# Kernel tuning notes

Measured on AMD Instinct MI355X. Metric: run time of the kernel, lower is better.

The kernel has to match this reference:

```python
import jax, jax.numpy as jnp
import numpy as np

B, N, DIM = 4, 2048, 768
H, C = 12, 64            # num_heads, head_dim
M = 384                  # num random features = dim * kernel_ratio
SCALE = C ** (-0.25)
EPS = 1e-8
INV_SQRT_M = 1.0 / np.sqrt(M).astype(np.float32)


def _make_orf(key):
    # per-head orthogonal random features: rows of each (C, M) block are
    # orthonormal (C <= M), scaled by sqrt(M), matching sample_orf's intent.
    g = jax.random.normal(key, (H, M, C), jnp.float32)
    q = jnp.linalg.qr(g)[0]                 # (H, M, C), orthonormal columns
    return jnp.transpose(q, (0, 2, 1)) * np.float32(np.sqrt(M))  # (H, C, M)


def setup_inputs() -> dict:
    key = jax.random.key(0)
    k0, k1, k2, k3 = jax.random.split(key, 4)
    x = jax.random.normal(k0, (B, N, DIM), jnp.float32)
    w = _make_orf(k1)                                       # (H, C, M), frozen
    Wqkv = jax.random.normal(k2, (DIM, 3 * DIM), jnp.float32) * 0.02
    Wproj = jax.random.normal(k3, (DIM, DIM), jnp.float32) * 0.02
    bproj = jnp.zeros((DIM,), jnp.float32)
    return {"x": x, "w": w, "Wqkv": Wqkv, "Wproj": Wproj, "bproj": bproj}


def _kernel(x, w):
    # x: (B, H, N, C) -> phi(x): (B, H, N, M)
    xs = x * SCALE
    proj = jnp.einsum('bhnc,hcm->bhnm', xs, w)
    sq_half = 0.5 * jnp.sum(xs * xs, axis=-1, keepdims=True)  # (B,H,N,1)
    return jnp.exp(proj - sq_half) * INV_SQRT_M


def reference(x, w, Wqkv, Wproj, bproj):
    qkv = (x @ Wqkv).reshape(B, N, 3, H, C).transpose(2, 0, 3, 1, 4)
    q, k, v = qkv[0], qkv[1], qkv[2]
    qf = _kernel(q, w)                       # (B, H, N, M)
    kf = _kernel(k, w)                       # (B, H, N, M)
    # normalizer D_n = q'_n . sum_j k'_j
    D = jnp.einsum('bhnm,bhm->bhn', qf, jnp.sum(kf, axis=2)) + EPS
    # linear attention: (k'^T v) then q' @ (k'^T v)
    ktv = jnp.einsum('bhnm,bhnc->bhmc', kf, v)      # (B, H, M, C)
    out = jnp.einsum('bhnm,bhmc->bhnc', qf, ktv) / D[..., None]
    out = out.transpose(0, 2, 1, 3).reshape(B, N, DIM)
    return out @ Wproj + bproj
```

## Files before the change

### kernel.cpp

```cpp
#include <hip/hip_runtime.h>

typedef __attribute__((ext_vector_type(8))) short s16x8;
typedef __attribute__((ext_vector_type(4))) float f32x4;

#define MFMA(a, b, c) __builtin_amdgcn_mfma_f32_16x16x32_bf16(a, b, c, 0, 0, 0)

namespace {

constexpr int Bn = 4, Nn = 2048, Hn = 12, Mn = 384;
constexpr float SCALE = 0.35355339059327379f;
constexpr float ISM = 0.05103103630798288f;
constexpr float EPS = 1e-8f;

__device__ inline unsigned short f2b(float f) {
  unsigned u = __builtin_bit_cast(unsigned, f);
  return (unsigned short)((u + 0x7fffu + ((u >> 16) & 1u)) >> 16);
}
__device__ inline float b2f(unsigned short h) {
  unsigned u = ((unsigned)h) << 16;
  return __builtin_bit_cast(float, u);
}

__device__ inline void gl_lds16(const unsigned short* g, unsigned short* l) {
  __builtin_amdgcn_global_load_lds(
      (const __attribute__((address_space(1))) unsigned int*)g,
      (__attribute__((address_space(3))) unsigned int*)l, 16, 0, 0);
}

__global__ __launch_bounds__(256) void cvt_all_k(const float* __restrict__ x,
                                                 const float* __restrict__ Wqkv,
                                                 const float* __restrict__ Wproj,
                                                 const float* __restrict__ w,
                                                 unsigned short* __restrict__ xb,
                                                 unsigned short* __restrict__ wqT,
                                                 unsigned short* __restrict__ wpT,
                                                 unsigned short* __restrict__ wt) {
  const int bid = blockIdx.x;
  if (bid < 3072) {
    const int id = bid * 256 + threadIdx.x;
    const float* src = x + (size_t)id * 8;
    s16x8 o;
#pragma unroll
    for (int j = 0; j < 8; ++j) o[j] = (short)f2b(src[j]);
    *(s16x8*)(xb + (size_t)id * 8) = o;
  } else if (bid < 3936) {
    const int id = (bid - 3072) * 256 + threadIdx.x;
    const int n = id / 96, kc = (id % 96) * 8;
    s16x8 o;
#pragma unroll
    for (int j = 0; j < 8; ++j) o[j] = (short)f2b(Wqkv[(size_t)(kc + j) * 2304 + n]);
    *(s16x8*)(wqT + (size_t)n * 768 + kc) = o;
  } else if (bid < 4224) {
    const int id = (bid - 3936) * 256 + threadIdx.x;
    const int n = id / 96, kc = (id % 96) * 8;
    s16x8 o;
#pragma unroll
    for (int j = 0; j < 8; ++j) o[j] = (short)f2b(Wproj[(size_t)(kc + j) * 768 + n]);
    *(s16x8*)(wpT + (size_t)n * 768 + kc) = o;
  } else {
    const int id = (bid - 4224) * 256 + threadIdx.x;
    const int h = id / (384 * 8);
    const int r = id % (384 * 8);
    const int m = r / 8, cc = (r % 8) * 8;
    s16x8 o;
#pragma unroll
    for (int j = 0; j < 8; ++j) o[j] = (short)f2b(w[((size_t)h * 64 + cc + j) * 384 + m]);
    *(s16x8*)(wt + ((size_t)h * 384 + m) * 64 + cc) = o;
  }
}

template <bool BF16OUT>
__global__ __launch_bounds__(256) void gemm_bt_k(const unsigned short* __restrict__ A,
                                                 const unsigned short* __restrict__ Bt,
                                                 int Ktot, int ldOut,
                                                 unsigned short* __restrict__ obf,
                                                 float* __restrict__ of32,
                                                 const float* __restrict__ bias) {
  __shared__ unsigned short ldsA[2][128 * 64];
  __shared__ unsigned short ldsB[2][128 * 64];
  const int t = threadIdx.x, lane = t & 63, w = t >> 6;
  const int ln = lane & 15, kg = lane >> 4;
  const size_t bm = (size_t)blockIdx.y * 128, bn = (size_t)blockIdx.x * 128;
  const int wr = w >> 1, wc = w & 1;
  const int sr = lane >> 3, s = lane & 7;
  f32x4 acc[4][4];
#pragma unroll
  for (int i = 0; i < 4; ++i)
#pragma unroll
    for (int j = 0; j < 4; ++j) acc[i][j] = (f32x4){0.f, 0.f, 0.f, 0.f};

  auto stage = [&](int kb, int d) {
#pragma unroll
    for (int c = 0; c < 4; ++c) {
      const int row = c * 32 + w * 8 + sr;
      const int ss = (s ^ (row & 7)) * 8;
      gl_lds16(A + (bm + row) * 768 + kb + ss, &ldsA[d][(c * 4 + w) * 512]);
      gl_lds16(Bt + (bn + row) * 768 + kb + ss, &ldsB[d][(c * 4 + w) * 512]);
    }
  };

  const int nt = Ktot / 64;
  stage(0, 0);
  for (int ti = 0; ti < nt; ++ti) {
    const int cur = ti & 1;
    __syncthreads();
    if (ti + 1 < nt) stage((ti + 1) * 64, cur ^ 1);
    const char* lA = (const char*)ldsA[cur];
    const char* lB = (const char*)ldsB[cur];
#pragma unroll
    for (int ks = 0; ks < 2; ++ks) {
      s16x8 af[4], bfr[4];
#pragma unroll
      for (int mi = 0; mi < 4; ++mi) {
        const int row = wr * 64 + mi * 16 + ln;
        af[mi] = *(const s16x8*)(lA + row * 128 + (((ks * 4 + kg) ^ (row & 7)) << 4));
      }
#pragma unroll
      for (int ni = 0; ni < 4; ++ni) {
        const int row = wc * 64 + ni * 16 + ln;
        bfr[ni] = *(const s16x8*)(lB + row * 128 + (((ks * 4 + kg) ^ (row & 7)) << 4));
      }
#pragma unroll
      for (int mi = 0; mi < 4; ++mi)
#pragma unroll
        for (int ni = 0; ni < 4; ++ni) acc[mi][ni] = MFMA(af[mi], bfr[ni], acc[mi][ni]);
    }
  }
#pragma unroll
  for (int mi = 0; mi < 4; ++mi)
#pragma unroll
    for (int ni = 0; ni < 4; ++ni) {
      const size_t orow0 = bm + wr * 64 + mi * 16 + kg * 4;
      const size_t ocol = bn + wc * 64 + ni * 16 + ln;
#pragma unroll
      for (int r = 0; r < 4; ++r) {
        const float v = acc[mi][ni][r];
        if (BF16OUT)
          obf[(orow0 + r) * ldOut + ocol] = f2b(v);
        else
          of32[(orow0 + r) * ldOut + ocol] = v + bias[ocol];
      }
    }
}

template <int NCT, int CT0>
__device__ inline void s2_gemm2(const char* kfT_b, const char* vt_b, int mts, int ln, int kg,
                                f32x4 (*acc)[3]) {
#pragma unroll
  for (int half = 0; half < 2; ++half) {
    s16x8 a[3], bb[NCT];
#pragma unroll
    for (int j = 0; j < 3; ++j) {
      const int m = (mts + j) * 16 + ln;
      a[j] = *(const s16x8*)(kfT_b + m * 128 + ((half * 64 + kg * 16) ^ ((m & 7) << 4)));
    }
#pragma unroll
    for (int i = 0; i < NCT; ++i) {
      const int c = (CT0 + i) * 16 + ln;
      bb[i] = *(const s16x8*)(vt_b + c * 128 + ((half * 64 + kg * 16) ^ ((c & 7) << 4)));
    }
#pragma unroll
    for (int j = 0; j < 3; ++j)
#pragma unroll
      for (int i = 0; i < NCT; ++i) acc[j][i] = MFMA(a[j], bb[i], acc[j][i]);
  }
}

__global__ __launch_bounds__(512, 4) void stage2_k(const unsigned short* __restrict__ qkv,
                                                   const unsigned short* __restrict__ wt,
                                                   float* __restrict__ ktv_part,
                                                   float* __restrict__ ksum_part) {
  __shared__ unsigned short kfT[192 * 64];
  __shared__ unsigned short vt[80 * 64];
  __shared__ unsigned short wt_s[192 * 64];
  __shared__ unsigned short k_s[64 * 64];
  __shared__ float sqh[64];
  char* kfT_b = (char*)kfT;
  char* vt_b = (char*)vt;
  char* wt_b = (char*)wt_s;
  char* k_b = (char*)k_s;
  const int t = threadIdx.x, lane = t & 63, w = t >> 6;
  const int ln = lane & 15, kg = lane >> 4;
  const int gx = blockIdx.x, h = blockIdx.y, b = blockIdx.z;
  const int ng = gx >> 1, mh = gx & 1, m0 = mh * 192;
  const int bh = b * Hn + h;
  const int ntile = w & 3, mgrp = w >> 2;
  const int mts = (w & 3) * 3;
  const int cg = w >> 2;
  const int lr = lane >> 3, sl = lane & 7;

  auto stage_k = [&](int ch) {
    const int row = w * 8 + lr;
    gl_lds16(qkv + ((size_t)b * Nn + ng * 512 + ch * 64 + row) * 2304 + 768 + h * 64 +
                 ((sl ^ (row & 7)) * 8),
             k_s + w * 512);
  };
  const int vn = t >> 3, vc0 = (t & 7) * 8;
  auto load_v = [&](int ch) {
    return *(const s16x8*)(qkv + ((size_t)b * Nn + ng * 512 + ch * 64 + vn) * 2304 + 1536 +
                           h * 64 + vc0);
  };
  auto scat_v = [&](s16x8 vv) {
#pragma unroll
    for (int j = 0; j < 8; ++j) {
      const int c = vc0 + j;
      *(unsigned short*)(vt_b + c * 128 + ((2 * vn) ^ ((c & 7) << 4))) = (unsigned short)vv[j];
    }
  };
  auto do_sq = [&]() {
    const int n = t >> 3, slq = t & 7;
    const s16x8 kk = *(const s16x8*)(k_b + n * 128 + ((slq ^ (n & 7)) << 4));
    float sacc = 0.f;
#pragma unroll
    for (int j = 0; j < 8; ++j) {
      const float f = b2f((unsigned short)kk[j]);
      sacc = fmaf(f, f, sacc);
    }
    sacc += __shfl_xor(sacc, 1);
    sacc += __shfl_xor(sacc, 2);
    sacc += __shfl_xor(sacc, 4);
    if ((t & 7) == 0) sqh[n] = 0.5f * SCALE * SCALE * sacc;
  };

#pragma unroll
  for (int rr = 0; rr < 3; ++rr) {
    const int j = w * 3 + rr;
    const int row = j * 8 + lr;
    gl_lds16(wt + ((size_t)h * 384 + m0 + row) * 64 + ((sl ^ (row & 7)) * 8), wt_s + j * 512);
  }
  for (int i = t; i < 1024; i += 512) {
    const int c = 64 + (i >> 6), nn = i & 63;
    *(unsigned short*)(vt_b + c * 128 + ((2 * nn) ^ ((c & 7) << 4))) =
        (c == 64) ? (unsigned short)0x3F80 : (unsigned short)0;
  }
  stage_k(0);
  s16x8 vreg = load_v(0);
  __syncthreads();
  scat_v(vreg);
  do_sq();
  __syncthreads();

  f32x4 acc[3][3];
#pragma unroll
  for (int j = 0; j < 3; ++j)
#pragma unroll
    for (int i = 0; i < 3; ++i) acc[j][i] = (f32x4){0.f, 0.f, 0.f, 0.f};

  for (int ch = 0; ch < 8; ++ch) {
    {
      const int arow = ntile * 16 + ln;
      const s16x8 a0 = *(const s16x8*)(k_b + arow * 128 + ((kg ^ (arow & 7)) << 4));
      const s16x8 a1 = *(const s16x8*)(k_b + arow * 128 + (((kg + 4) ^ (arow & 7)) << 4));
      const int nr = ntile * 16 + kg * 4;
      const float s0 = sqh[nr], s1 = sqh[nr + 1], s2 = sqh[nr + 2], s3 = sqh[nr + 3];
#pragma unroll
      for (int i = 0; i < 6; ++i) {
        const int mloc = (mgrp * 6 + i) * 16 + ln;
        const s16x8 b0 = *(const s16x8*)(wt_b + mloc * 128 + ((kg ^ (mloc & 7)) << 4));
        const s16x8 b1 = *(const s16x8*)(wt_b + mloc * 128 + (((kg + 4) ^ (mloc & 7)) << 4));
        f32x4 p = (f32x4){0.f, 0.f, 0.f, 0.f};
        p = MFMA(a0, b0, p);
        p = MFMA(a1, b1, p);
        const float e0 = __expf(fmaf(SCALE, p[0], -s0)) * ISM;
        const float e1 = __expf(fmaf(SCALE, p[1], -s1)) * ISM;
        const float e2 = __expf(fmaf(SCALE, p[2], -s2)) * ISM;
        const float e3 = __expf(fmaf(SCALE, p[3], -s3)) * ISM;
        uint2 pk;
        pk.x = (unsigned)f2b(e0) | ((unsigned)f2b(e1) << 16);
        pk.y = (unsigned)f2b(e2) | ((unsigned)f2b(e3) << 16);
        const int bytn = 32 * ntile + 8 * kg;
        *(uint2*)(kfT_b + mloc * 128 + (bytn ^ ((mloc & 7) << 4))) = pk;
      }
    }
    __syncthreads();
    if (ch < 7) {
      stage_k(ch + 1);
      vreg = load_v(ch + 1);
    }
    if (cg == 0)
      s2_gemm2<3, 0>(kfT_b, vt_b, mts, ln, kg, acc);
    else
      s2_gemm2<2, 3>(kfT_b, vt_b, mts, ln, kg, acc);
    __syncthreads();
    if (ch < 7) {
      scat_v(vreg);
      do_sq();
      __syncthreads();
    }
  }
  float* base = ktv_part + ((size_t)ng * 48 + bh) * (384 * 64);
  const int nct2 = cg ? 2 : 3, ct0c = cg ? 3 : 0;
#pragma unroll
  for (int j = 0; j < 3; ++j)
#pragma unroll
    for (int i = 0; i < 3; ++i) {
      if (i >= nct2) continue;
      const int ct = ct0c + i;
      const int mrow0 = m0 + (mts + j) * 16 + kg * 4;
      if (ct < 4) {
        const int c = ct * 16 + ln;
#pragma unroll
        for (int r = 0; r < 4; ++r) base[(size_t)(mrow0 + r) * 64 + c] = acc[j][i][r];
      } else if (ln == 0) {
#pragma unroll
        for (int r = 0; r < 4; ++r)
          ksum_part[((size_t)ng * 48 + bh) * 384 + mrow0 + r] = acc[j][i][r];
      }
    }
}

__global__ __launch_bounds__(256) void reduce_all_k(const float* __restrict__ part,
                                                    const float* __restrict__ partk,
                                                    unsigned short* __restrict__ ktve) {
  const int bid = blockIdx.x;
  if (bid < 4608) {
    const int bh = bid / 96, chunk = bid % 96;
    const int idx = chunk * 256 + threadIdx.x;
    const int m = idx >> 6, c = idx & 63;
    const size_t o = (size_t)bh * 24576 + idx;
    const size_t gs = (size_t)48 * 24576;
    const float s = part[o] + part[o + gs] + part[o + 2 * gs] + part[o + 3 * gs];
    ktve[((size_t)bh * 80 + c) * 384 + m] = f2b(s);
  } else {
    const int idx = (bid - 4608) * 256 + threadIdx.x;
    const int bh = idx / 384, m = idx % 384;
    const int gs = 48 * 384;
    const float s = partk[idx] + partk[idx + gs] + partk[idx + 2 * gs] + partk[idx + 3 * gs];
    const unsigned short hi = f2b(s);
    const unsigned short lo = f2b(s - b2f(hi));
    const size_t base = ((size_t)bh * 80 + 64) * 384 + m;
    ktve[base] = hi;
    ktve[base + 384] = lo;
  }
}

__global__ __launch_bounds__(512, 4) void stage3_k(const unsigned short* __restrict__ qkv,
                                                   const unsigned short* __restrict__ wt,
                                                   const unsigned short* __restrict__ ktve,
                                                   unsigned short* __restrict__ attn) {
  __shared__ unsigned short q_s[128 * 64];
  __shared__ unsigned short qf_s[128 * 64];
  __shared__ unsigned short wt_s[2][64 * 64];
  __shared__ unsigned short kt_s[2][80 * 64];
  char* q_b = (char*)q_s;
  char* qf_b = (char*)qf_s;
  const int t = threadIdx.x, lane = t & 63, w = t >> 6;
  const int ln = lane & 15, kg = lane >> 4;
  const int nb = blockIdx.x, h = blockIdx.y, b = blockIdx.z, bh = b * Hn + h;
  const size_t tok0 = (size_t)b * Nn + nb * 128;
  const int lr = lane >> 3, sl = lane & 7;

#pragma unroll
  for (int rr = 0; rr < 2; ++rr) {
    const int row = w * 16 + rr * 8 + lr;
    gl_lds16(qkv + (tok0 + row) * 2304 + h * 64 + ((sl ^ (row & 7)) * 8),
             q_s + (w * 16 + rr * 8) * 64 + lane * 8);
  }
  auto stage_wt = [&](int mc, int pb) {
    const int row = w * 8 + lr;
    gl_lds16(wt + ((size_t)h * 384 + mc * 64 + row) * 64 + ((sl ^ (row & 7)) * 8),
             wt_s[pb] + w * 512 + lane * 8);
  };
  auto stage_kt = [&](int mc, int pb) {
    const int row = w * 8 + lr;
    gl_lds16(ktve + ((size_t)bh * 80 + row) * 384 + mc * 64 + ((sl ^ (row & 7)) * 8),
             kt_s[pb] + w * 512 + lane * 8);
    if (w < 2) {
      const int row2 = 64 + w * 8 + lr;
      gl_lds16(ktve + ((size_t)bh * 80 + row2) * 384 + mc * 64 + ((sl ^ (row2 & 7)) * 8),
               kt_s[pb] + (64 + w * 8) * 64 + lane * 8);
    }
  };
  stage_wt(0, 0);
  stage_kt(0, 0);
  __syncthreads();

  f32x4 acc2[5];
#pragma unroll
  for (int i = 0; i < 5; ++i) acc2[i] = (f32x4){0.f, 0.f, 0.f, 0.f};

  const int arow = w * 16 + ln;
  const char* qrow = q_b + arow * 128;
  const int asw = (arow & 7) << 4;

  for (int mc = 0; mc < 6; ++mc) {
    const int pb = mc & 1;
    if (mc < 5) {
      stage_wt(mc + 1, pb ^ 1);
      stage_kt(mc + 1, pb ^ 1);
    }
    const s16x8 af0 = *(const s16x8*)(qrow + ((kg << 4) ^ asw));
    const s16x8 af1 = *(const s16x8*)(qrow + (((kg + 4) << 4) ^ asw));
    const char* wb = (const char*)wt_s[pb];
    f32x4 p[4];
#pragma unroll
    for (int mt = 0; mt < 4; ++mt) {
      const int mrow = mt * 16 + ln;
      const s16x8 b0 = *(const s16x8*)(wb + mrow * 128 + ((kg ^ (mrow & 7)) << 4));
      const s16x8 b1 = *(const s16x8*)(wb + mrow * 128 + (((kg + 4) ^ (mrow & 7)) << 4));
      f32x4 pp = (f32x4){0.f, 0.f, 0.f, 0.f};
      pp = MFMA(af0, b0, pp);
      p[mt] = MFMA(af1, b1, pp);
    }
#pragma unroll
    for (int mt = 0; mt < 4; ++mt) {
#pragma unroll
      for (int r = 0; r < 4; ++r) {
        const int trow = w * 16 + kg * 4 + r;
        const int m = mt * 16 + ln;
        *(unsigned short*)(qf_b + trow * 128 + ((2 * m) ^ ((trow & 7) << 4))) =
            f2b(__expf(SCALE * p[mt][r]));
      }
    }
    const char* qfr = qf_b + arow * 128;
    const s16x8 a0 = *(const s16x8*)(qfr + ((kg << 4) ^ asw));
    const s16x8 a1 = *(const s16x8*)(qfr + (((kg + 4) << 4) ^ asw));
    const char* kb = (const char*)kt_s[pb];
#pragma unroll
    for (int ct = 0; ct < 5; ++ct) {
      const int crow = ct * 16 + ln;
      const s16x8 b0 = *(const s16x8*)(kb + crow * 128 + ((kg ^ (crow & 7)) << 4));
      const s16x8 b1 = *(const s16x8*)(kb + crow * 128 + (((kg + 4) ^ (crow & 7)) << 4));
      acc2[ct] = MFMA(a0, b0, acc2[ct]);
      acc2[ct] = MFMA(a1, b1, acc2[ct]);
    }
    __syncthreads();
  }
  float dv[4];
#pragma unroll
  for (int r = 0; r < 4; ++r) {
    const float hi = __shfl(acc2[4][r], (lane & 48));
    const float lo = __shfl(acc2[4][r], (lane & 48) | 1);
    dv[r] = 1.0f / (hi + lo + EPS);
  }
#pragma unroll
  for (int ct = 0; ct < 4; ++ct) {
#pragma unroll
    for (int r = 0; r < 4; ++r) {
      const int trow = w * 16 + kg * 4 + r;
      const int c = ct * 16 + ln;
      attn[(tok0 + trow) * 768 + h * 64 + c] = f2b(acc2[ct][r] * dv[r]);
    }
  }
}

}

extern "C" void kernel_launch(void* const* d_in, const int* in_sizes, int n_in,
                              void* d_out, int out_size, void* d_ws, size_t ws_size,
                              hipStream_t stream) {
  const float* x = (const float*)d_in[0];
  const float* w = (const float*)d_in[1];
  const float* Wqkv = (const float*)d_in[2];
  const float* Wproj = (const float*)d_in[3];
  const float* bproj = (const float*)d_in[4];

  char* ws = (char*)d_ws;
  unsigned short* xb = (unsigned short*)(ws);
  unsigned short* wqT = (unsigned short*)(ws + 12582912);
  float* ktv_part = (float*)(ws);
  float* ksum_part = (float*)(ws + 18874368);
  char* p = ws + 19169280;
  unsigned short* qkvb = (unsigned short*)p;  p += 37748736;
  unsigned short* wt = (unsigned short*)p;    p += 589824;
  unsigned short* ktve = (unsigned short*)p;  p += 2949120;
  unsigned short* attn = (unsigned short*)p;  p += 12582912;
  unsigned short* wpT = (unsigned short*)p;

  cvt_all_k<<<4368, 256, 0, stream>>>(x, Wqkv, Wproj, w, xb, wqT, wpT, wt);
  gemm_bt_k<true><<<dim3(18, 64), 256, 0, stream>>>(xb, wqT, 768, 2304, qkvb, nullptr, nullptr);
  stage2_k<<<dim3(8, 12, 4), 512, 0, stream>>>(qkvb, wt, ktv_part, ksum_part);
  reduce_all_k<<<4680, 256, 0, stream>>>(ktv_part, ksum_part, ktve);
  stage3_k<<<dim3(16, 12, 4), 512, 0, stream>>>(qkvb, wt, ktve, attn);
  gemm_bt_k<false><<<dim3(6, 64), 256, 0, stream>>>(attn, wpT, 768, 768, nullptr,
                                                    (float*)d_out, bproj);
}
```

Baseline: 158.0 us.

## Split GEMM into specialized QKV and projection kernels with block swizzle and single buffering

Replaces the templated double-buffered GEMM with two specialized kernels. Both use single-buffered LDS with two barriers per K step, which cuts LDS use and may raise occupancy, and both remap block indices in an XCD-style swizzle to improve L2 locality. The projection GEMM switches to 128x64 tiles, doubling its grid from 384 to 768 blocks to fill more CUs. The cost is losing the overlap of global loads with MFMA compute that double buffering provided.

New measurement: 149.6 us. -5.3%, faster.

```diff
diff --git a/kernel.cpp b/kernel.cpp
--- a/kernel.cpp
+++ b/kernel.cpp
@@ -69,18 +69,18 @@
   }
 }
 
-template <bool BF16OUT>
-__global__ __launch_bounds__(256) void gemm_bt_k(const unsigned short* __restrict__ A,
-                                                 const unsigned short* __restrict__ Bt,
-                                                 int Ktot, int ldOut,
-                                                 unsigned short* __restrict__ obf,
-                                                 float* __restrict__ of32,
-                                                 const float* __restrict__ bias) {
-  __shared__ unsigned short ldsA[2][128 * 64];
-  __shared__ unsigned short ldsB[2][128 * 64];
+__global__ __launch_bounds__(256) void gemm_qkv_k(const unsigned short* __restrict__ A,
+                                                  const unsigned short* __restrict__ Bt,
+                                                  unsigned short* __restrict__ obf) {
+  __shared__ unsigned short ldsA[128 * 64];
+  __shared__ unsigned short ldsB[128 * 64];
+  char* lA = (char*)ldsA;
+  char* lB = (char*)ldsB;
   const int t = threadIdx.x, lane = t & 63, w = t >> 6;
   const int ln = lane & 15, kg = lane >> 4;
-  const size_t bm = (size_t)blockIdx.y * 128, bn = (size_t)blockIdx.x * 128;
+  const int flat = blockIdx.y * 18 + blockIdx.x;
+  const int swz = (flat & 7) * 144 + (flat >> 3);
+  const size_t bm = (size_t)(swz / 18) * 128, bn = (size_t)(swz % 18) * 128;
   const int wr = w >> 1, wc = w & 1;
   const int sr = lane >> 3, s = lane & 7;
   f32x4 acc[4][4];
@@ -89,24 +89,16 @@
 #pragma unroll
     for (int j = 0; j < 4; ++j) acc[i][j] = (f32x4){0.f, 0.f, 0.f, 0.f};
 
-  auto stage = [&](int kb, int d) {
+  for (int kb = 0; kb < 768; kb += 64) {
+    __syncthreads();
 #pragma unroll
     for (int c = 0; c < 4; ++c) {
       const int row = c * 32 + w * 8 + sr;
       const int ss = (s ^ (row & 7)) * 8;
-      gl_lds16(A + (bm + row) * 768 + kb + ss, &ldsA[d][(c * 4 + w) * 512]);
-      gl_lds16(Bt + (bn + row) * 768 + kb + ss, &ldsB[d][(c * 4 + w) * 512]);
-    }
-  };
-
-  const int nt = Ktot / 64;
-  stage(0, 0);
-  for (int ti = 0; ti < nt; ++ti) {
-    const int cur = ti & 1;
-    __syncthreads();
-    if (ti + 1 < nt) stage((ti + 1) * 64, cur ^ 1);
-    const char* lA = (const char*)ldsA[cur];
-    const char* lB = (const char*)ldsB[cur];
+      gl_lds16(A + (bm + row) * 768 + kb + ss, ldsA + (c * 4 + w) * 512);
+      gl_lds16(Bt + (bn + row) * 768 + kb + ss, ldsB + (c * 4 + w) * 512);
+    }
+    __syncthreads();
 #pragma unroll
     for (int ks = 0; ks < 2; ++ks) {
       s16x8 af[4], bfr[4];
@@ -133,13 +125,74 @@
       const size_t orow0 = bm + wr * 64 + mi * 16 + kg * 4;
       const size_t ocol = bn + wc * 64 + ni * 16 + ln;
 #pragma unroll
-      for (int r = 0; r < 4; ++r) {
-        const float v = acc[mi][ni][r];
-        if (BF16OUT)
-          obf[(orow0 + r) * ldOut + ocol] = f2b(v);
-        else
-          of32[(orow0 + r) * ldOut + ocol] = v + bias[ocol];
-      }
+      for (int r = 0; r < 4; ++r) obf[(orow0 + r) * 2304 + ocol] = f2b(acc[mi][ni][r]);
+    }
+}
+
+__global__ __launch_bounds__(256) void gemm_proj_k(const unsigned short* __restrict__ A,
+                                                   const unsigned short* __restrict__ Bt,
+                                                   float* __restrict__ out,
+                                                   const float* __restrict__ bias) {
+  __shared__ unsigned short ldsA[128 * 64];
+  __shared__ unsigned short ldsB[64 * 64];
+  char* lA = (char*)ldsA;
+  char* lB = (char*)ldsB;
+  const int t = threadIdx.x, lane = t & 63, w = t >> 6;
+  const int ln = lane & 15, kg = lane >> 4;
+  const int flat = blockIdx.y * 12 + blockIdx.x;
+  const int swz = (flat & 7) * 96 + (flat >> 3);
+  const size_t bm = (size_t)(swz / 12) * 128, bn = (size_t)(swz % 12) * 64;
+  const int wr = w >> 1, wc = w & 1;
+  const int sr = lane >> 3, s = lane & 7;
+  f32x4 acc[4][2];
+#pragma unroll
+  for (int i = 0; i < 4; ++i)
+#pragma unroll
+    for (int j = 0; j < 2; ++j) acc[i][j] = (f32x4){0.f, 0.f, 0.f, 0.f};
+
+  for (int kb = 0; kb < 768; kb += 64) {
+    __syncthreads();
+#pragma unroll
+    for (int c = 0; c < 4; ++c) {
+      const int row = c * 32 + w * 8 + sr;
+      const int ss = (s ^ (row & 7)) * 8;
+      gl_lds16(A + (bm + row) * 768 + kb + ss, ldsA + (c * 4 + w) * 512);
+    }
+#pragma unroll
+    for (int c = 0; c < 2; ++c) {
+      const int row = c * 32 + w * 8 + sr;
+      const int ss = (s ^ (row & 7)) * 8;
+      gl_lds16(Bt + (bn + row) * 768 + kb + ss, ldsB + (c * 4 + w) * 512);
+    }
+    __syncthreads();
+#pragma unroll
+    for (int ks = 0; ks < 2; ++ks) {
+      s16x8 af[4], bfr[2];
+#pragma unroll
+      for (int mi = 0; mi < 4; ++mi) {
+        const int row = wr * 64 + mi * 16 + ln;
+        af[mi] = *(const s16x8*)(lA + row * 128 + (((ks * 4 + kg) ^ (row & 7)) << 4));
+      }
+#pragma unroll
+      for (int ni = 0; ni < 2; ++ni) {
+        const int row = wc * 32 + ni * 16 + ln;
+        bfr[ni] = *(const s16x8*)(lB + row * 128 + (((ks * 4 + kg) ^ (row & 7)) << 4));
+      }
+#pragma unroll
+      for (int mi = 0; mi < 4; ++mi)
+#pragma unroll
+        for (int ni = 0; ni < 2; ++ni) acc[mi][ni] = MFMA(af[mi], bfr[ni], acc[mi][ni]);
+    }
+  }
+#pragma unroll
+  for (int mi = 0; mi < 4; ++mi)
+#pragma unroll
+    for (int ni = 0; ni < 2; ++ni) {
+      const size_t orow0 = bm + wr * 64 + mi * 16 + kg * 4;
+      const size_t ocol = bn + wc * 32 + ni * 16 + ln;
+      const float bv = bias[ocol];
+#pragma unroll
+      for (int r = 0; r < 4; ++r) out[(orow0 + r) * 768 + ocol] = acc[mi][ni][r] + bv;
     }
 }
 
@@ -468,10 +521,9 @@
   unsigned short* wpT = (unsigned short*)p;
 
   cvt_all_k<<<4368, 256, 0, stream>>>(x, Wqkv, Wproj, w, xb, wqT, wpT, wt);
-  gemm_bt_k<true><<<dim3(18, 64), 256, 0, stream>>>(xb, wqT, 768, 2304, qkvb, nullptr, nullptr);
+  gemm_qkv_k<<<dim3(18, 64), 256, 0, stream>>>(xb, wqT, qkvb);
   stage2_k<<<dim3(8, 12, 4), 512, 0, stream>>>(qkvb, wt, ktv_part, ksum_part);
   reduce_all_k<<<4680, 256, 0, stream>>>(ktv_part, ksum_part, ktve);
   stage3_k<<<dim3(16, 12, 4), 512, 0, stream>>>(qkvb, wt, ktve, attn);
-  gemm_bt_k<false><<<dim3(6, 64), 256, 0, stream>>>(attn, wpT, 768, 768, nullptr,
-                                                    (float*)d_out, bproj);
-}
+  gemm_proj_k<<<dim3(12, 64), 256, 0, stream>>>(attn, wpT, (float*)d_out, bproj);
+}
```
